# Kernel tuning notes

Hardware: AMD Instinct MI355X
Metric: run time of the kernel (lower is better)

## Reference

```python
import jax, jax.numpy as jnp
import numpy as np

N_NODES = 50000
N_EDGES = 800000
IN_DIM = 6
HID = 256
OUT = 256
N_EXPERTS = 8
N_LAYERS = 2
N_GRAPHS = 64


def setup_inputs() -> dict:
    key = jax.random.key(0)
    ks = jax.random.split(key, 16)
    s = 0.05
    x = jax.random.normal(ks[0], (N_NODES, IN_DIM), dtype=jnp.float32)
    edge_index = jax.random.randint(ks[1], (2, N_EDGES), 0, N_NODES, dtype=jnp.int64)
    batch = jnp.sort(jax.random.randint(ks[2], (N_NODES,), 0, N_GRAPHS, dtype=jnp.int64))
    # shared encoder
    W_enc = jax.random.normal(ks[3], (IN_DIM, HID), jnp.float32) * s
    b_enc = jnp.zeros((HID,), jnp.float32)
    # router MLP: (HID+2) -> HID -> N_EXPERTS
    Wr1 = jax.random.normal(ks[4], (HID + 2, HID), jnp.float32) * s
    br1 = jnp.zeros((HID,), jnp.float32)
    Wr2 = jax.random.normal(ks[5], (HID, N_EXPERTS), jnp.float32) * s
    br2 = jnp.zeros((N_EXPERTS,), jnp.float32)
    # experts: 2 GraphConv layers each (self weight + neighbor weight + bias), stacked over experts
    Ws0 = jax.random.normal(ks[6], (N_EXPERTS, HID, HID), jnp.float32) * s
    Wn0 = jax.random.normal(ks[7], (N_EXPERTS, HID, HID), jnp.float32) * s
    b0 = jnp.zeros((N_EXPERTS, HID), jnp.float32)
    Ws1 = jax.random.normal(ks[8], (N_EXPERTS, HID, OUT), jnp.float32) * s
    Wn1 = jax.random.normal(ks[9], (N_EXPERTS, HID, OUT), jnp.float32) * s
    b1 = jnp.zeros((N_EXPERTS, OUT), jnp.float32)
    return dict(x=x, edge_index=edge_index, batch=batch, W_enc=W_enc, b_enc=b_enc,
                Wr1=Wr1, br1=br1, Wr2=Wr2, br2=br2,
                Ws0=Ws0, Wn0=Wn0, b0=b0, Ws1=Ws1, Wn1=Wn1, b1=b1)


def _graph_conv(h, src, dst, Ws, Wn, b):
    # PyG GraphConv: x' = x @ Ws + sum_{j in N(i)} x_j @ Wn + b
    msg = h[src] @ Wn                                   # [E, d_out]
    agg = jax.ops.segment_sum(msg, dst, num_segments=N_NODES)
    return h @ Ws + agg + b


def reference(x, edge_index, batch, W_enc, b_enc, Wr1, br1, Wr2, br2,
              Ws0, Wn0, b0, Ws1, Wn1, b1):
    src, dst = edge_index[0], edge_index[1]
    # shared encoder
    h = jax.nn.relu(x @ W_enc + b_enc)                  # [N, HID]
    # graph size features: per-graph node count and edge count, log-scaled, broadcast to nodes
    ones_n = jnp.ones((h.shape[0],), h.dtype)
    node_cnt = jax.ops.segment_sum(ones_n, batch, num_segments=N_GRAPHS)
    edge_cnt = jax.ops.segment_sum(jnp.ones((src.shape[0],), h.dtype), batch[src], num_segments=N_GRAPHS)
    size_feat = jnp.stack([jnp.log1p(node_cnt)[batch], jnp.log1p(edge_cnt)[batch]], axis=-1)  # [N, 2]
    # router -> top-1 expert index
    r = jax.nn.relu(jnp.concatenate([h, size_feat], axis=-1) @ Wr1 + br1)
    logits = r @ Wr2 + br2                              # [N, n_experts]
    idx = jnp.argmax(logits, axis=-1)                   # [N]
    # dense compute-all-experts, then gather by argmax (faithful to original)
    out = jnp.zeros((h.shape[0], Ws1.shape[-1]), h.dtype)
    for e in range(N_EXPERTS):
        z = jax.nn.relu(_graph_conv(h, src, dst, Ws0[e], Wn0[e], b0[e]))
        y_e = _graph_conv(z, src, dst, Ws1[e], Wn1[e], b1[e])   # [N, OUT]
        out = out + jnp.where((idx == e)[:, None], y_e, 0.0)
    return out
```

## Files before the change

kernel.cpp:

```cpp
#include <hip/hip_runtime.h>
#include <hip/hip_bf16.h>
#include <math.h>

#define NN 50000
#define NE 800000
#define NG 64
#define NEXP 8

typedef __attribute__((ext_vector_type(8))) short bf16x8;
typedef __attribute__((ext_vector_type(4))) float f32x4;
typedef unsigned short ushort_t;

__device__ __forceinline__ unsigned short f2bf(float f) {
  union { float f; unsigned u; } x; x.f = f;
  unsigned r = x.u + 0x7fff + ((x.u >> 16) & 1);
  return (unsigned short)(r >> 16);
}
__device__ __forceinline__ float bf2f(unsigned short u) {
  union { unsigned u; float f; } x; x.u = ((unsigned)u) << 16; return x.f;
}

__device__ __forceinline__ void gld16(const void* g, void* l) {
  __builtin_amdgcn_global_load_lds(
      (const __attribute__((address_space(1))) unsigned int*)g,
      (__attribute__((address_space(3))) unsigned int*)l, 16, 0, 0);
}

__global__ __launch_bounds__(256) void k_encoder(
    const float* __restrict__ x, const float* __restrict__ W,
    const float* __restrict__ b, ushort_t* __restrict__ Xb,
    ushort_t* __restrict__ Xlo) {
  int i = blockIdx.x, n = threadIdx.x;
  float acc = b[n];
#pragma unroll
  for (int k = 0; k < 6; k++) acc = fmaf(x[i * 6 + k], W[k * 256 + n], acc);
  acc = fmaxf(acc, 0.f);
  unsigned short hb = f2bf(acc);
  Xb[(size_t)i * 512 + n] = hb;
  Xlo[(size_t)i * 256 + n] = f2bf(acc - bf2f(hb));
}

__global__ __launch_bounds__(256) void k_count_nodes(
    const int* __restrict__ batch, int* __restrict__ node_cnt) {
  __shared__ int bins[NG];
  int t = threadIdx.x;
  if (t < NG) bins[t] = 0;
  __syncthreads();
  for (int i = blockIdx.x * blockDim.x + t; i < NN; i += gridDim.x * blockDim.x)
    atomicAdd(&bins[batch[i]], 1);
  __syncthreads();
  if (t < NG) atomicAdd(&node_cnt[t], bins[t]);
}

__global__ __launch_bounds__(256) void k_count_edges(
    const int* __restrict__ ei, const int* __restrict__ batch,
    int* __restrict__ edge_cnt, int* __restrict__ deg) {
  __shared__ int bins[NG];
  int t = threadIdx.x;
  if (t < NG) bins[t] = 0;
  __syncthreads();
  for (int e = blockIdx.x * blockDim.x + t; e < NE; e += gridDim.x * blockDim.x) {
    int s = ei[e];
    int d = ei[NE + e];
    atomicAdd(&bins[batch[s]], 1);
    atomicAdd(&deg[d], 1);
  }
  __syncthreads();
  if (t < NG) atomicAdd(&edge_cnt[t], bins[t]);
}

__global__ __launch_bounds__(256) void k_sizefeat(
    const int* __restrict__ batch, const int* __restrict__ node_cnt,
    const int* __restrict__ edge_cnt, float* __restrict__ sf0,
    float* __restrict__ sf1) {
  int i = blockIdx.x * blockDim.x + threadIdx.x;
  if (i < NN) {
    int g = batch[i];
    sf0[i] = log1pf((float)node_cnt[g]);
    sf1[i] = log1pf((float)edge_cnt[g]);
  }
}

__global__ __launch_bounds__(1024) void k_scan(
    const int* __restrict__ deg, int* __restrict__ offs, int* __restrict__ cursor) {
  __shared__ int wsums[16];
  int t = threadIdx.x, lane = t & 63, wid = t >> 6;
  int carry = 0;
  for (int base = 0; base < NN; base += 1024) {
    int i = base + t;
    int v = (i < NN) ? deg[i] : 0;
    int x = v;
#pragma unroll
    for (int d = 1; d < 64; d <<= 1) {
      int y = __shfl_up(x, d, 64);
      if (lane >= d) x += y;
    }
    if (lane == 63) wsums[wid] = x;
    __syncthreads();
    if (wid == 0) {
      int s = (lane < 16) ? wsums[lane] : 0;
#pragma unroll
      for (int d = 1; d < 16; d <<= 1) {
        int y = __shfl_up(s, d, 64);
        if (lane >= d) s += y;
      }
      if (lane < 16) wsums[lane] = s;
    }
    __syncthreads();
    int wpre = (wid > 0) ? wsums[wid - 1] : 0;
    int excl = carry + wpre + x - v;
    if (i < NN) { offs[i] = excl; cursor[i] = excl; }
    int btot = wsums[15];
    __syncthreads();
    carry += btot;
  }
  if (t == 0) offs[NN] = carry;
}

__global__ __launch_bounds__(256) void k_fill_csr(
    const int* __restrict__ ei, int* __restrict__ cursor, int* __restrict__ edge_src) {
  int e = blockIdx.x * blockDim.x + threadIdx.x;
  if (e < NE) {
    int d = ei[NE + e];
    int pos = atomicAdd(&cursor[d], 1);
    edge_src[pos] = ei[e];
  }
}

__global__ __launch_bounds__(256) void k_agg_h2(
    const int* __restrict__ offs, const int* __restrict__ edge_src,
    ushort_t* __restrict__ Xb) {
  int wid = threadIdx.x >> 6, lane = threadIdx.x & 63;
  int half = lane >> 5, cl = lane & 31;
  int i = blockIdx.x * 4 + wid;
  if (i >= NN) return;
  int e0 = offs[i], e1 = offs[i + 1];
  float acc[8] = {};
  int k = e0;
  for (; k + 8 <= e1; k += 8) {
    int s0 = edge_src[k + half];
    int s1 = edge_src[k + 2 + half];
    int s2 = edge_src[k + 4 + half];
    int s3 = edge_src[k + 6 + half];
    bf16x8 v0 = *(const bf16x8*)&Xb[(size_t)s0 * 512 + cl * 8];
    bf16x8 v1 = *(const bf16x8*)&Xb[(size_t)s1 * 512 + cl * 8];
    bf16x8 v2 = *(const bf16x8*)&Xb[(size_t)s2 * 512 + cl * 8];
    bf16x8 v3 = *(const bf16x8*)&Xb[(size_t)s3 * 512 + cl * 8];
#pragma unroll
    for (int j = 0; j < 8; j++) acc[j] += bf2f((unsigned short)v0[j]);
#pragma unroll
    for (int j = 0; j < 8; j++) acc[j] += bf2f((unsigned short)v1[j]);
#pragma unroll
    for (int j = 0; j < 8; j++) acc[j] += bf2f((unsigned short)v2[j]);
#pragma unroll
    for (int j = 0; j < 8; j++) acc[j] += bf2f((unsigned short)v3[j]);
  }
  for (; k + 2 <= e1; k += 2) {
    int s0 = edge_src[k + half];
    bf16x8 v0 = *(const bf16x8*)&Xb[(size_t)s0 * 512 + cl * 8];
#pragma unroll
    for (int j = 0; j < 8; j++) acc[j] += bf2f((unsigned short)v0[j]);
  }
  if (k < e1 && half == 0) {
    int s0 = edge_src[k];
    bf16x8 v0 = *(const bf16x8*)&Xb[(size_t)s0 * 512 + cl * 8];
#pragma unroll
    for (int j = 0; j < 8; j++) acc[j] += bf2f((unsigned short)v0[j]);
  }
#pragma unroll
  for (int j = 0; j < 8; j++) acc[j] += __shfl_xor(acc[j], 32, 64);
  if (half == 0) {
    bf16x8 o;
#pragma unroll
    for (int j = 0; j < 8; j++) o[j] = (short)f2bf(acc[j]);
    *(bf16x8*)(&Xb[(size_t)i * 512 + 256 + cl * 8]) = o;
  }
}

__global__ __launch_bounds__(256) void k_prep_w(
    const float* __restrict__ Ws0, const float* __restrict__ Wn0,
    const float* __restrict__ Ws1, const float* __restrict__ Wn1,
    ushort_t* __restrict__ Wt1, ushort_t* __restrict__ Wt2) {
  __shared__ float tile[32][33];
  int z = blockIdx.z;
  int e = z & 7;
  const float* Ws = (z < 8) ? Ws0 : Ws1;
  const float* Wn = (z < 8) ? Wn0 : Wn1;
  ushort_t* Wt = (z < 8) ? Wt1 : Wt2;
  int kt = blockIdx.x;
  int nt = blockIdx.y;
  int tx = threadIdx.x & 31, ty = threadIdx.x >> 5;
  const float* src = (kt < 8) ? (Ws + e * 65536 + (kt * 32) * 256)
                              : (Wn + e * 65536 + ((kt - 8) * 32) * 256);
#pragma unroll
  for (int rr = 0; rr < 32; rr += 8) {
    int k = rr + ty;
    tile[k][tx] = src[k * 256 + nt * 32 + tx];
  }
  __syncthreads();
#pragma unroll
  for (int rr = 0; rr < 32; rr += 8) {
    int n = rr + ty;
    Wt[(size_t)e * 131072 + (nt * 32 + n) * 512 + kt * 32 + tx] = f2bf(tile[tx][n]);
  }
}

__global__ __launch_bounds__(256) void k_prep_wr1(
    const float* __restrict__ Wr1, ushort_t* __restrict__ Wr1t) {
  int k = blockIdx.x;
  int n = threadIdx.x;
  unsigned short v;
  if (k < 256) {
    v = f2bf(Wr1[k * 256 + n]);
  } else {
    float f = Wr1[(k - 256) * 256 + n];
    unsigned short h = f2bf(f);
    v = f2bf(f - bf2f(h));
  }
  Wr1t[(size_t)n * 512 + k] = v;
}

#define TIE_TAU 1e-4f
__global__ __launch_bounds__(256) void k_router_mfma(
    const ushort_t* __restrict__ Xb,
    const ushort_t* __restrict__ Xlo,
    const ushort_t* __restrict__ Wr1t,
    const float* __restrict__ Wr1, const float* __restrict__ br1,
    const float* __restrict__ Wr2, const float* __restrict__ sf0,
    const float* __restrict__ sf1, float* __restrict__ Lpart) {
  __shared__ ushort_t As[2][4096];
  __shared__ ushort_t Bs1[2][4096];
  __shared__ ushort_t Bs2[2][4096];
  __shared__ float Lsm[128][NEXP];
  int t = threadIdx.x;
  int w = t >> 6, lane = t & 63;
  int m0 = blockIdx.x * 128;
  int n0 = blockIdx.y * 128;
  int wm = w >> 1, wn = w & 1;
  for (int z = t; z < 128 * NEXP; z += 256) ((float*)Lsm)[z] = 0.f;

  auto STAGE = [&](int s, int kt) {
    int k0 = (kt & 7) * 32;
    bool hi = kt < 8;
#pragma unroll
    for (int i = 0; i < 2; i++) {
      int c = w * 128 + i * 64 + lane;
      int r = c >> 2, kc = c & 3;
      int gr = m0 + r; if (gr >= NN) gr = NN - 1;
      int dst = (w * 128 + i * 64) * 8;
      if (hi) {
        gld16(Xb + (size_t)gr * 512 + k0 + kc * 8, (void*)&As[s][dst]);
        gld16(Wr1t + (size_t)(n0 + r) * 512 + k0 + kc * 8, (void*)&Bs1[s][dst]);
        gld16(Wr1t + (size_t)(n0 + r) * 512 + 256 + k0 + kc * 8, (void*)&Bs2[s][dst]);
      } else {
        gld16(Xlo + (size_t)gr * 256 + k0 + kc * 8, (void*)&As[s][dst]);
        gld16(Wr1t + (size_t)(n0 + r) * 512 + k0 + kc * 8, (void*)&Bs1[s][dst]);
      }
    }
  };

  f32x4 acc[4][4] = {};
  STAGE(0, 0);
  __syncthreads();
  for (int kt = 0; kt < 16; kt++) {
    int cur = kt & 1;
    if (kt < 15) STAGE(cur ^ 1, kt + 1);
    bf16x8 a[4], b1[4];
#pragma unroll
    for (int i = 0; i < 4; i++) {
      int ra = wm * 64 + i * 16 + (lane & 15);
      a[i] = *(const bf16x8*)&As[cur][ra * 32 + (lane >> 4) * 8];
      int nb = wn * 64 + i * 16 + (lane & 15);
      b1[i] = *(const bf16x8*)&Bs1[cur][nb * 32 + (lane >> 4) * 8];
    }
#pragma unroll
    for (int i = 0; i < 4; i++)
#pragma unroll
      for (int j = 0; j < 4; j++)
        acc[i][j] = __builtin_amdgcn_mfma_f32_16x16x32_bf16(a[i], b1[j], acc[i][j], 0, 0, 0);
    if (kt < 8) {
      bf16x8 b2[4];
#pragma unroll
      for (int i = 0; i < 4; i++) {
        int nb = wn * 64 + i * 16 + (lane & 15);
        b2[i] = *(const bf16x8*)&Bs2[cur][nb * 32 + (lane >> 4) * 8];
      }
#pragma unroll
      for (int i = 0; i < 4; i++)
#pragma unroll
        for (int j = 0; j < 4; j++)
          acc[i][j] = __builtin_amdgcn_mfma_f32_16x16x32_bf16(a[i], b2[j], acc[i][j], 0, 0, 0);
    }
    __syncthreads();
  }

  int q = lane >> 4, c15 = lane & 15;
  float bb[4], w6[4], w7[4];
#pragma unroll
  for (int j = 0; j < 4; j++) {
    int col = n0 + wn * 64 + j * 16 + c15;
    bb[j] = br1[col];
    w6[j] = Wr1[65536 + col];
    w7[j] = Wr1[65792 + col];
  }
#pragma unroll
  for (int i = 0; i < 4; i++)
#pragma unroll
    for (int v = 0; v < 4; v++) {
      int row = m0 + wm * 64 + i * 16 + q * 4 + v;
      float s0v = (row < NN) ? sf0[row] : 0.f;
      float s1v = (row < NN) ? sf1[row] : 0.f;
#pragma unroll
      for (int j = 0; j < 4; j++)
        acc[i][j][v] = fmaxf(acc[i][j][v] + bb[j] + s0v * w6[j] + s1v * w7[j], 0.f);
    }
#pragma unroll
  for (int e = 0; e < NEXP; e++) {
    float wr2j[4];
#pragma unroll
    for (int j = 0; j < 4; j++)
      wr2j[j] = Wr2[(n0 + wn * 64 + j * 16 + c15) * 8 + e];
    float pe[4][4];
#pragma unroll
    for (int i = 0; i < 4; i++)
#pragma unroll
      for (int v = 0; v < 4; v++) {
        float s = acc[i][0][v] * wr2j[0];
        s = fmaf(acc[i][1][v], wr2j[1], s);
        s = fmaf(acc[i][2][v], wr2j[2], s);
        s = fmaf(acc[i][3][v], wr2j[3], s);
        pe[i][v] = s;
      }
#pragma unroll
    for (int d = 1; d < 16; d <<= 1)
#pragma unroll
      for (int i = 0; i < 4; i++)
#pragma unroll
        for (int v = 0; v < 4; v++)
          pe[i][v] += __shfl_xor(pe[i][v], d, 64);
    if (c15 == 0) {
#pragma unroll
      for (int i = 0; i < 4; i++)
#pragma unroll
        for (int v = 0; v < 4; v++)
          atomicAdd(&Lsm[wm * 64 + i * 16 + q * 4 + v][e], pe[i][v]);
    }
  }
  __syncthreads();
  for (int z = t; z < 128 * NEXP; z += 256) {
    int lr = z >> 3, e = z & 7;
    int row = m0 + lr;
    if (row < NN)
      Lpart[(size_t)blockIdx.y * NN * 8 + (size_t)row * 8 + e] = Lsm[lr][e];
  }
}

__global__ __launch_bounds__(256) void k_argmax(
    const float* __restrict__ Lpart, const float* __restrict__ br2,
    int* __restrict__ idx, int* __restrict__ nfix, int* __restrict__ fixlist) {
  int i = blockIdx.x * 256 + threadIdx.x;
  if (i >= NN) return;
  float best = -1e30f, second = -1e30f; int bi = 0;
#pragma unroll
  for (int e = 0; e < NEXP; e++) {
    float v = Lpart[(size_t)i * 8 + e] + Lpart[(size_t)NN * 8 + (size_t)i * 8 + e]
              + br2[e];
    if (v > best) { second = best; best = v; bi = e; }
    else if (v > second) second = v;
  }
  idx[i] = bi;
  if (best - second < TIE_TAU) {
    int p = atomicAdd(nfix, 1);
    fixlist[p] = i;
  }
}

__global__ __launch_bounds__(256) void k_fixup(
    const float* __restrict__ x, const float* __restrict__ W_enc,
    const float* __restrict__ b_enc, const float* __restrict__ Wr1,
    const float* __restrict__ br1, const float* __restrict__ Wr2,
    const float* __restrict__ br2, const float* __restrict__ sf0,
    const float* __restrict__ sf1, const int* __restrict__ fixlist,
    const int* __restrict__ nfix, int* __restrict__ idx) {
  __shared__ float hsh[256];
  __shared__ float lred[4][NEXP];
  int n = *nfix;
  int t = threadIdx.x, wid = t >> 6, lane = t & 63;
  for (int qq = blockIdx.x; qq < n; qq += gridDim.x) {
    int node = fixlist[qq];
    float hv = b_enc[t];
#pragma unroll
    for (int k = 0; k < 6; k++)
      hv = fmaf(x[node * 6 + k], W_enc[k * 256 + t], hv);
    hsh[t] = fmaxf(hv, 0.f);
    __syncthreads();
    float acc = br1[t] + sf0[node] * Wr1[65536 + t] + sf1[node] * Wr1[65792 + t];
    for (int k = 0; k < 256; k++)
      acc = fmaf(hsh[k], Wr1[k * 256 + t], acc);
    float r = fmaxf(acc, 0.f);
    float le[NEXP];
#pragma unroll
    for (int e = 0; e < NEXP; e++) le[e] = r * Wr2[t * 8 + e];
#pragma unroll
    for (int d = 32; d > 0; d >>= 1)
#pragma unroll
      for (int e = 0; e < NEXP; e++) le[e] += __shfl_xor(le[e], d, 64);
    if (lane == 0) {
#pragma unroll
      for (int e = 0; e < NEXP; e++) lred[wid][e] = le[e];
    }
    __syncthreads();
    if (t == 0) {
      float best = -1e30f; int bi = 0;
      for (int e = 0; e < NEXP; e++) {
        float v = lred[0][e] + lred[1][e] + lred[2][e] + lred[3][e] + br2[e];
        if (v > best) { best = v; bi = e; }
      }
      idx[node] = bi;
    }
    __syncthreads();
  }
}

__global__ __launch_bounds__(256) void k_ecnt(
    const int* __restrict__ idx, int* __restrict__ ecnt) {
  __shared__ int bins[NEXP];
  int t = threadIdx.x;
  if (t < NEXP) bins[t] = 0;
  __syncthreads();
  for (int i = blockIdx.x * 256 + t; i < NN; i += gridDim.x * 256)
    atomicAdd(&bins[idx[i]], 1);
  __syncthreads();
  if (t < NEXP) atomicAdd(&ecnt[t], bins[t]);
}

__global__ __launch_bounds__(256) void k_srcmask(
    const int* __restrict__ ei, const int* __restrict__ idx,
    unsigned int* __restrict__ mask) {
  int k = blockIdx.x * 256 + threadIdx.x;
  if (k < NE) {
    int s = ei[k], d = ei[NE + k];
    atomicOr(&mask[s], 1u << idx[d]);
  }
  if (k < NN) atomicOr(&mask[k], 1u << idx[k]);
}

__global__ __launch_bounds__(256) void k_scount(
    const unsigned int* __restrict__ mask, int* __restrict__ scnt) {
  __shared__ int bins[NEXP];
  int t = threadIdx.x;
  if (t < NEXP) bins[t] = 0;
  __syncthreads();
  for (int i = blockIdx.x * 256 + t; i < NN; i += gridDim.x * 256) {
    unsigned m = mask[i];
    while (m) { int b = __ffs(m) - 1; atomicAdd(&bins[b], 1); m &= m - 1; }
  }
  __syncthreads();
  if (t < NEXP) atomicAdd(&scnt[t], bins[t]);
}

__global__ void k_bucket_offs(const int* __restrict__ ecnt,
                              const int* __restrict__ scnt,
                              int* __restrict__ boff, int* __restrict__ bcur,
                              int* __restrict__ tstart,
                              int* __restrict__ soff, int* __restrict__ scur) {
  if (threadIdx.x == 0) {
    int s = 0, ts = 0, s2 = 0;
    for (int e = 0; e < NEXP; e++) {
      boff[e] = s; bcur[e] = s;
      tstart[e] = ts;
      ts += (ecnt[e] + 127) / 128;
      s += ecnt[e];
      soff[e] = s2; scur[e] = s2;
      s2 += scnt[e];
    }
    boff[NEXP] = s;
    tstart[NEXP] = ts;
    soff[NEXP] = s2;
  }
}

#define BF_BLOCKS 64
__global__ __launch_bounds__(256) void k_bucket_fill2(
    const int* __restrict__ idx, int* __restrict__ bcur, int* __restrict__ nlist) {
  __shared__ int lcnt[NEXP];
  __shared__ int lbase[NEXP];
  int t = threadIdx.x;
  int chunk = (NN + BF_BLOCKS - 1) / BF_BLOCKS;
  int lo = blockIdx.x * chunk;
  int hi = lo + chunk; if (hi > NN) hi = NN;
  if (t < NEXP) lcnt[t] = 0;
  __syncthreads();
  for (int i = lo + t; i < hi; i += 256) atomicAdd(&lcnt[idx[i]], 1);
  __syncthreads();
  if (t < NEXP) lbase[t] = atomicAdd(&bcur[t], lcnt[t]);
  __syncthreads();
  if (t < NEXP) lcnt[t] = 0;
  __syncthreads();
  for (int i = lo + t; i < hi; i += 256) {
    int e = idx[i];
    int p = atomicAdd(&lcnt[e], 1);
    nlist[lbase[e] + p] = i;
  }
}

__global__ __launch_bounds__(256) void k_scompact(
    const unsigned int* __restrict__ mask, int* __restrict__ scur,
    int* __restrict__ slist) {
  __shared__ int lcnt[NEXP];
  __shared__ int lbase[NEXP];
  int t = threadIdx.x;
  int chunk = (NN + BF_BLOCKS - 1) / BF_BLOCKS;
  int lo = blockIdx.x * chunk;
  int hi = lo + chunk; if (hi > NN) hi = NN;
  if (t < NEXP) lcnt[t] = 0;
  __syncthreads();
  for (int i = lo + t; i < hi; i += 256) {
    unsigned m = mask[i];
    while (m) { int b = __ffs(m) - 1; atomicAdd(&lcnt[b], 1); m &= m - 1; }
  }
  __syncthreads();
  if (t < NEXP) lbase[t] = atomicAdd(&scur[t], lcnt[t]);
  __syncthreads();
  if (t < NEXP) lcnt[t] = 0;
  __syncthreads();
  for (int i = lo + t; i < hi; i += 256) {
    unsigned m = mask[i];
    while (m) {
      int b = __ffs(m) - 1;
      int p = atomicAdd(&lcnt[b], 1);
      slist[lbase[b] + p] = i;
      m &= m - 1;
    }
  }
}

__global__ __launch_bounds__(256) void k_layer1_rows(
    const ushort_t* __restrict__ Abf,
    const ushort_t* __restrict__ Wt,
    const float* __restrict__ b0, const int* __restrict__ idx,
    const int* __restrict__ slist, const int* __restrict__ soff, int e,
    ushort_t* __restrict__ Zb, ushort_t* __restrict__ A2) {
  int base = soff[e];
  int cnt = soff[e + 1] - base;
  int m0 = blockIdx.x * 128;
  if (m0 >= cnt) return;
  __shared__ ushort_t As[2][4096];
  __shared__ ushort_t Bs[2][4096];
  __shared__ int rows[128];
  __shared__ int sidx[128];
  int t = threadIdx.x;
  if (t < 128) {
    int r = (m0 + t < cnt) ? slist[base + m0 + t] : -1;
    rows[t] = r;
    sidx[t] = (r >= 0) ? idx[r] : -1;
  }
  __syncthreads();
  int w = t >> 6, lane = t & 63;
  int n0 = blockIdx.y * 128;
  int wm = w >> 1, wn = w & 1;
  const ushort_t* Wb = Wt + (size_t)e * 131072;

  auto STAGE = [&](int s, int kt) {
    int k0 = kt * 32;
#pragma unroll
    for (int i = 0; i < 2; i++) {
      int c = w * 128 + i * 64 + lane;
      int r = c >> 2, kc = c & 3;
      int nd = rows[r]; if (nd < 0) nd = 0;
      int dst = (w * 128 + i * 64) * 8;
      gld16(Abf + (size_t)nd * 512 + k0 + kc * 8, (void*)&As[s][dst]);
      gld16(Wb + (size_t)(n0 + r) * 512 + k0 + kc * 8, (void*)&Bs[s][dst]);
    }
  };

  f32x4 acc[4][4] = {};
  STAGE(0, 0);
  __syncthreads();
  for (int kt = 0; kt < 16; kt++) {
    int cur = kt & 1;
    if (kt < 15) STAGE(cur ^ 1, kt + 1);
    bf16x8 a[4], b[4];
#pragma unroll
    for (int i = 0; i < 4; i++) {
      int ra = wm * 64 + i * 16 + (lane & 15);
      a[i] = *(const bf16x8*)&As[cur][ra * 32 + (lane >> 4) * 8];
      int nb = wn * 64 + i * 16 + (lane & 15);
      b[i] = *(const bf16x8*)&Bs[cur][nb * 32 + (lane >> 4) * 8];
    }
#pragma unroll
    for (int i = 0; i < 4; i++)
#pragma unroll
      for (int j = 0; j < 4; j++)
        acc[i][j] = __builtin_amdgcn_mfma_f32_16x16x32_bf16(a[i], b[j], acc[i][j], 0, 0, 0);
    __syncthreads();
  }
  int q = lane >> 4, c15 = lane & 15;
#pragma unroll
  for (int i = 0; i < 4; i++) {
#pragma unroll
    for (int j = 0; j < 4; j++) {
      int col = n0 + wn * 64 + j * 16 + c15;
      float bias = b0[e * 256 + col];
#pragma unroll
      for (int v = 0; v < 4; v++) {
        int lrow = wm * 64 + i * 16 + q * 4 + v;
        int node = rows[lrow];
        if (node >= 0) {
          unsigned short zb = f2bf(fmaxf(acc[i][j][v] + bias, 0.f));
          Zb[(size_t)node * 256 + col] = zb;
          if (sidx[lrow] == e) A2[(size_t)node * 512 + col] = zb;
        }
      }
    }
  }
}

__global__ __launch_bounds__(256) void k_agg_z2(
    const ushort_t* __restrict__ Zb, const int* __restrict__ offs,
    const int* __restrict__ edge_src, const int* __restrict__ nlist,
    const int* __restrict__ boff, int e, ushort_t* __restrict__ A2) {
  int wid = threadIdx.x >> 6, lane = threadIdx.x & 63;
  int half = lane >> 5, cl = lane & 31;
  int base = boff[e];
  int cnt = boff[e + 1] - base;
  for (int b = blockIdx.x * 4 + wid; b < cnt; b += gridDim.x * 4) {
    int i = nlist[base + b];
    int e0 = offs[i], e1 = offs[i + 1];
    float acc[8] = {};
    int k = e0;
    for (; k + 8 <= e1; k += 8) {
      int s0 = edge_src[k + half];
      int s1 = edge_src[k + 2 + half];
      int s2 = edge_src[k + 4 + half];
      int s3 = edge_src[k + 6 + half];
      bf16x8 v0 = *(const bf16x8*)&Zb[(size_t)s0 * 256 + cl * 8];
      bf16x8 v1 = *(const bf16x8*)&Zb[(size_t)s1 * 256 + cl * 8];
      bf16x8 v2 = *(const bf16x8*)&Zb[(size_t)s2 * 256 + cl * 8];
      bf16x8 v3 = *(const bf16x8*)&Zb[(size_t)s3 * 256 + cl * 8];
#pragma unroll
      for (int j = 0; j < 8; j++) acc[j] += bf2f((unsigned short)v0[j]);
#pragma unroll
      for (int j = 0; j < 8; j++) acc[j] += bf2f((unsigned short)v1[j]);
#pragma unroll
      for (int j = 0; j < 8; j++) acc[j] += bf2f((unsigned short)v2[j]);
#pragma unroll
      for (int j = 0; j < 8; j++) acc[j] += bf2f((unsigned short)v3[j]);
    }
    for (; k + 2 <= e1; k += 2) {
      int s0 = edge_src[k + half];
      bf16x8 v0 = *(const bf16x8*)&Zb[(size_t)s0 * 256 + cl * 8];
#pragma unroll
      for (int j = 0; j < 8; j++) acc[j] += bf2f((unsigned short)v0[j]);
    }
    if (k < e1 && half == 0) {
      int s0 = edge_src[k];
      bf16x8 v0 = *(const bf16x8*)&Zb[(size_t)s0 * 256 + cl * 8];
#pragma unroll
      for (int j = 0; j < 8; j++) acc[j] += bf2f((unsigned short)v0[j]);
    }
#pragma unroll
    for (int j = 0; j < 8; j++) acc[j] += __shfl_xor(acc[j], 32, 64);
    if (half == 0) {
      bf16x8 o;
#pragma unroll
      for (int j = 0; j < 8; j++) o[j] = (short)f2bf(acc[j]);
      *(bf16x8*)(&A2[(size_t)i * 512 + 256 + cl * 8]) = o;
    }
  }
}

#define MAXT2 (391 + NEXP)
__global__ __launch_bounds__(256) void k_layer2_mfma(
    const ushort_t* __restrict__ A2,
    const ushort_t* __restrict__ Wt,
    const float* __restrict__ b1, const int* __restrict__ nlist,
    const int* __restrict__ boff, const int* __restrict__ tstart,
    float* __restrict__ outp) {
  __shared__ ushort_t As[2][4096];
  __shared__ ushort_t Bs[2][4096];
  __shared__ int rows[128];
  int t = threadIdx.x;
  int tx = blockIdx.x;
  int e = -1;
#pragma unroll
  for (int q = 0; q < NEXP; q++)
    if (tx >= tstart[q] && tx < tstart[q + 1]) e = q;
  if (e < 0) return;
  int tile = tx - tstart[e];
  int base = boff[e];
  int cnt = boff[e + 1] - base;
  int m0 = tile * 128;
  if (t < 128) rows[t] = (m0 + t < cnt) ? nlist[base + m0 + t] : -1;
  __syncthreads();
  int w = t >> 6, lane = t & 63;
  int n0 = blockIdx.y * 128;
  int wm = w >> 1, wn = w & 1;
  const ushort_t* Wb = Wt + (size_t)e * 131072;

  auto STAGE = [&](int s, int kt) {
    int k0 = kt * 32;
#pragma unroll
    for (int i = 0; i < 2; i++) {
      int c = w * 128 + i * 64 + lane;
      int r = c >> 2, kc = c & 3;
      int nd = rows[r]; if (nd < 0) nd = 0;
      int dst = (w * 128 + i * 64) * 8;
      gld16(A2 + (size_t)nd * 512 + k0 + kc * 8, (void*)&As[s][dst]);
      gld16(Wb + (size_t)(n0 + r) * 512 + k0 + kc * 8, (void*)&Bs[s][dst]);
    }
  };

  f32x4 acc[4][4] = {};
  STAGE(0, 0);
  __syncthreads();
  for (int kt = 0; kt < 16; kt++) {
    int cur = kt & 1;
    if (kt < 15) STAGE(cur ^ 1, kt + 1);
    bf16x8 a[4], b[4];
#pragma unroll
    for (int i = 0; i < 4; i++) {
      int ra = wm * 64 + i * 16 + (lane & 15);
      a[i] = *(const bf16x8*)&As[cur][ra * 32 + (lane >> 4) * 8];
      int nb = wn * 64 + i * 16 + (lane & 15);
      b[i] = *(const bf16x8*)&Bs[cur][nb * 32 + (lane >> 4) * 8];
    }
#pragma unroll
    for (int i = 0; i < 4; i++)
#pragma unroll
      for (int j = 0; j < 4; j++)
        acc[i][j] = __builtin_amdgcn_mfma_f32_16x16x32_bf16(a[i], b[j], acc[i][j], 0, 0, 0);
    __syncthreads();
  }
  int q = lane >> 4, c15 = lane & 15;
#pragma unroll
  for (int i = 0; i < 4; i++) {
#pragma unroll
    for (int j = 0; j < 4; j++) {
      int col = n0 + wn * 64 + j * 16 + c15;
      float bias = b1[e * 256 + col];
#pragma unroll
      for (int v = 0; v < 4; v++) {
        int lrow = wm * 64 + i * 16 + q * 4 + v;
        int node = rows[lrow];
        if (node >= 0) outp[(size_t)node * 256 + col] = acc[i][j][v] + bias;
      }
    }
  }
}

static inline char* wsalloc(char*& p, size_t bytes) {
  char* r = p;
  p += (bytes + 255) & ~(size_t)255;
  return r;
}

extern "C" void kernel_launch(void* const* d_in, const int* in_sizes, int n_in,
                              void* d_out, int out_size, void* d_ws, size_t ws_size,
                              hipStream_t stream) {
  const float* x     = (const float*)d_in[0];
  const int*   ei    = (const int*)d_in[1];
  const int*   batch = (const int*)d_in[2];
  const float* W_enc = (const float*)d_in[3];
  const float* b_enc = (const float*)d_in[4];
  const float* Wr1   = (const float*)d_in[5];
  const float* br1   = (const float*)d_in[6];
  const float* Wr2   = (const float*)d_in[7];
  const float* br2   = (const float*)d_in[8];
  const float* Ws0   = (const float*)d_in[9];
  const float* Wn0   = (const float*)d_in[10];
  const float* b0    = (const float*)d_in[11];
  const float* Ws1   = (const float*)d_in[12];
  const float* Wn1   = (const float*)d_in[13];
  const float* b1    = (const float*)d_in[14];
  float* outp = (float*)d_out;

  char* p = (char*)d_ws;
  ushort_t* Xb   = (ushort_t*)wsalloc(p, (size_t)NN * 512 * 2);
  ushort_t* Zb   = (ushort_t*)wsalloc(p, (size_t)NN * 256 * 2);
  ushort_t* A2   = (ushort_t*)wsalloc(p, (size_t)NN * 512 * 2);
  ushort_t* Xlo  = Zb;
  float*    Lpart= (float*)wsalloc(p, (size_t)2 * NN * 8 * 4);
  ushort_t* Wt1  = (ushort_t*)wsalloc(p, (size_t)NEXP * 256 * 512 * 2);
  ushort_t* Wt2  = (ushort_t*)wsalloc(p, (size_t)NEXP * 256 * 512 * 2);
  ushort_t* Wr1t = (ushort_t*)wsalloc(p, (size_t)256 * 512 * 2);
  int* edge_src  = (int*)wsalloc(p, (size_t)NE * 4);
  int* offs      = (int*)wsalloc(p, (size_t)(NN + 1) * 4);
  int* cursor    = (int*)wsalloc(p, (size_t)NN * 4);
  int* deg       = (int*)wsalloc(p, (size_t)NN * 4);
  int* idxb      = (int*)wsalloc(p, (size_t)NN * 4);
  float* sf0     = (float*)wsalloc(p, (size_t)NN * 4);
  float* sf1     = (float*)wsalloc(p, (size_t)NN * 4);
  int* nlist     = (int*)wsalloc(p, (size_t)NN * 4);
  int* fixlist   = (int*)wsalloc(p, (size_t)NN * 4);
  unsigned int* maskb = (unsigned int*)wsalloc(p, (size_t)NN * 4);
  int* slist     = (int*)wsalloc(p, (size_t)NN * NEXP * 4);
  int* smallb    = (int*)wsalloc(p, 256 * 4);
  int* node_cnt = smallb;
  int* edge_cnt = smallb + 64;
  int* ecnt     = smallb + 128;
  int* boff     = smallb + 136;
  int* bcur     = smallb + 152;
  int* tstart   = smallb + 160;
  int* nfix     = smallb + 192;
  int* scnt     = smallb + 200;
  int* soff     = smallb + 208;
  int* scur     = smallb + 224;

  hipMemsetAsync(deg, 0, (size_t)NN * 4, stream);
  hipMemsetAsync(smallb, 0, 256 * 4, stream);
  hipMemsetAsync(maskb, 0, (size_t)NN * 4, stream);

  k_encoder<<<NN, 256, 0, stream>>>(x, W_enc, b_enc, Xb, Xlo);
  k_count_nodes<<<64, 256, 0, stream>>>(batch, node_cnt);
  k_count_edges<<<128, 256, 0, stream>>>(ei, batch, edge_cnt, deg);
  k_sizefeat<<<(NN + 255) / 256, 256, 0, stream>>>(batch, node_cnt, edge_cnt, sf0, sf1);
  k_scan<<<1, 1024, 0, stream>>>(deg, offs, cursor);
  k_fill_csr<<<(NE + 255) / 256, 256, 0, stream>>>(ei, cursor, edge_src);
  k_agg_h2<<<(NN + 3) / 4, 256, 0, stream>>>(offs, edge_src, Xb);
  k_prep_w<<<dim3(16, 8, 16), 256, 0, stream>>>(Ws0, Wn0, Ws1, Wn1, Wt1, Wt2);
  k_prep_wr1<<<512, 256, 0, stream>>>(Wr1, Wr1t);
  k_router_mfma<<<dim3((NN + 127) / 128, 2), 256, 0, stream>>>(
      Xb, Xlo, Wr1t, Wr1, br1, Wr2, sf0, sf1, Lpart);
  k_argmax<<<(NN + 255) / 256, 256, 0, stream>>>(Lpart, br2, idxb, nfix, fixlist);
  k_fixup<<<256, 256, 0, stream>>>(x, W_enc, b_enc, Wr1, br1, Wr2, br2,
                                   sf0, sf1, fixlist, nfix, idxb);
  k_srcmask<<<(NE + 255) / 256, 256, 0, stream>>>(ei, idxb, maskb);
  k_ecnt<<<64, 256, 0, stream>>>(idxb, ecnt);
  k_scount<<<64, 256, 0, stream>>>(maskb, scnt);
  k_bucket_offs<<<1, 64, 0, stream>>>(ecnt, scnt, boff, bcur, tstart, soff, scur);
  k_bucket_fill2<<<BF_BLOCKS, 256, 0, stream>>>(idxb, bcur, nlist);
  k_scompact<<<BF_BLOCKS, 256, 0, stream>>>(maskb, scur, slist);
  for (int e = 0; e < NEXP; e++) {
    k_layer1_rows<<<dim3((NN + 127) / 128, 2), 256, 0, stream>>>(
        Xb, Wt1, b0, idxb, slist, soff, e, Zb, A2);
    k_agg_z2<<<3125, 256, 0, stream>>>(Zb, offs, edge_src, nlist, boff, e, A2);
  }
  k_layer2_mfma<<<dim3(MAXT2, 2), 256, 0, stream>>>(
      A2, Wt2, b1, nlist, boff, tstart, outp);
}
```

Baseline: 645.5 us.

## Restructure router GEMM: resident swizzled weight tile in LDS, A streamed from global

The router kernel now loads a full 64-column slice of the transposed router weight (all K) into LDS once, with an XOR swizzle to avoid bank conflicts. A-operand fragments are read directly from global memory into registers with software double-buffering, which removes the per-k-step LDS staging and barriers. The N split goes from 2 to 4 blocks, so each block does half the columns and argmax sums four partial logit buffers. This trades more redundant reads of the activation rows and a larger partial buffer for fewer syncs and more parallel blocks.

```diff
diff --git a/kernel.cpp b/kernel.cpp
--- a/kernel.cpp
+++ b/kernel.cpp
@@ -228,77 +228,95 @@
     const float* __restrict__ Wr1, const float* __restrict__ br1,
     const float* __restrict__ Wr2, const float* __restrict__ sf0,
     const float* __restrict__ sf1, float* __restrict__ Lpart) {
-  __shared__ ushort_t As[2][4096];
-  __shared__ ushort_t Bs1[2][4096];
-  __shared__ ushort_t Bs2[2][4096];
+  __shared__ ushort_t Bs[64 * 512];
   __shared__ float Lsm[128][NEXP];
   int t = threadIdx.x;
   int w = t >> 6, lane = t & 63;
   int m0 = blockIdx.x * 128;
-  int n0 = blockIdx.y * 128;
+  int n0 = blockIdx.y * 64;
   int wm = w >> 1, wn = w & 1;
+  int q16 = lane >> 4, c15 = lane & 15;
   for (int z = t; z < 128 * NEXP; z += 256) ((float*)Lsm)[z] = 0.f;
 
-  auto STAGE = [&](int s, int kt) {
-    int k0 = (kt & 7) * 32;
-    bool hi = kt < 8;
-#pragma unroll
-    for (int i = 0; i < 2; i++) {
-      int c = w * 128 + i * 64 + lane;
-      int r = c >> 2, kc = c & 3;
-      int gr = m0 + r; if (gr >= NN) gr = NN - 1;
-      int dst = (w * 128 + i * 64) * 8;
-      if (hi) {
-        gld16(Xb + (size_t)gr * 512 + k0 + kc * 8, (void*)&As[s][dst]);
-        gld16(Wr1t + (size_t)(n0 + r) * 512 + k0 + kc * 8, (void*)&Bs1[s][dst]);
-        gld16(Wr1t + (size_t)(n0 + r) * 512 + 256 + k0 + kc * 8, (void*)&Bs2[s][dst]);
-      } else {
-        gld16(Xlo + (size_t)gr * 256 + k0 + kc * 8, (void*)&As[s][dst]);
-        gld16(Wr1t + (size_t)(n0 + r) * 512 + k0 + kc * 8, (void*)&Bs1[s][dst]);
+#pragma unroll
+  for (int r = 0; r < 16; r++) {
+    int C0 = (r * 4 + w) * 64;
+    int C = C0 + lane;
+    int n = C >> 6, c = C & 63;
+    gld16(Wr1t + (size_t)(n0 + n) * 512 + ((c ^ (n & 7)) << 3),
+          (void*)((char*)Bs + (size_t)C0 * 16));
+  }
+
+  const ushort_t* pHi[4];
+  const ushort_t* pLo[4];
+#pragma unroll
+  for (int i = 0; i < 4; i++) {
+    int row = m0 + wm * 64 + i * 16 + c15;
+    if (row >= NN) row = NN - 1;
+    pHi[i] = Xb + (size_t)row * 512 + q16 * 8;
+    pLo[i] = Xlo + (size_t)row * 256 + q16 * 8;
+  }
+
+  f32x4 acc[4][2] = {};
+  __syncthreads();
+
+  auto LOADA_HI = [&](bf16x8* a, int kt) {
+#pragma unroll
+    for (int i = 0; i < 4; i++) a[i] = *(const bf16x8*)(pHi[i] + kt * 32);
+  };
+  auto LOADA_LO = [&](bf16x8* a, int kt) {
+#pragma unroll
+    for (int i = 0; i < 4; i++) a[i] = *(const bf16x8*)(pLo[i] + kt * 32);
+  };
+  auto MFMA_HI = [&](bf16x8* a, int kt) {
+#pragma unroll
+    for (int j = 0; j < 2; j++) {
+      int nb = wn * 32 + j * 16 + c15;
+      const char* brow = (const char*)Bs + nb * 1024;
+      int sw = nb & 7;
+      bf16x8 bh = *(const bf16x8*)(brow + (((kt * 4 + q16) ^ sw) << 4));
+      bf16x8 bl = *(const bf16x8*)(brow + (((32 + kt * 4 + q16) ^ sw) << 4));
+#pragma unroll
+      for (int i = 0; i < 4; i++) {
+        acc[i][j] = __builtin_amdgcn_mfma_f32_16x16x32_bf16(a[i], bh, acc[i][j], 0, 0, 0);
+        acc[i][j] = __builtin_amdgcn_mfma_f32_16x16x32_bf16(a[i], bl, acc[i][j], 0, 0, 0);
       }
     }
   };
-
-  f32x4 acc[4][4] = {};
-  STAGE(0, 0);
-  __syncthreads();
-  for (int kt = 0; kt < 16; kt++) {
-    int cur = kt & 1;
-    if (kt < 15) STAGE(cur ^ 1, kt + 1);
-    bf16x8 a[4], b1[4];
-#pragma unroll
-    for (int i = 0; i < 4; i++) {
-      int ra = wm * 64 + i * 16 + (lane & 15);
-      a[i] = *(const bf16x8*)&As[cur][ra * 32 + (lane >> 4) * 8];
-      int nb = wn * 64 + i * 16 + (lane & 15);
-      b1[i] = *(const bf16x8*)&Bs1[cur][nb * 32 + (lane >> 4) * 8];
-    }
-#pragma unroll
-    for (int i = 0; i < 4; i++)
-#pragma unroll
-      for (int j = 0; j < 4; j++)
-        acc[i][j] = __builtin_amdgcn_mfma_f32_16x16x32_bf16(a[i], b1[j], acc[i][j], 0, 0, 0);
-    if (kt < 8) {
-      bf16x8 b2[4];
-#pragma unroll
-      for (int i = 0; i < 4; i++) {
-        int nb = wn * 64 + i * 16 + (lane & 15);
-        b2[i] = *(const bf16x8*)&Bs2[cur][nb * 32 + (lane >> 4) * 8];
-      }
+  auto MFMA_LO = [&](bf16x8* a, int kt) {
+#pragma unroll
+    for (int j = 0; j < 2; j++) {
+      int nb = wn * 32 + j * 16 + c15;
+      const char* brow = (const char*)Bs + nb * 1024;
+      int sw = nb & 7;
+      bf16x8 bh = *(const bf16x8*)(brow + (((kt * 4 + q16) ^ sw) << 4));
 #pragma unroll
       for (int i = 0; i < 4; i++)
-#pragma unroll
-        for (int j = 0; j < 4; j++)
-          acc[i][j] = __builtin_amdgcn_mfma_f32_16x16x32_bf16(a[i], b2[j], acc[i][j], 0, 0, 0);
-    }
-    __syncthreads();
-  }
-
-  int q = lane >> 4, c15 = lane & 15;
-  float bb[4], w6[4], w7[4];
-#pragma unroll
-  for (int j = 0; j < 4; j++) {
-    int col = n0 + wn * 64 + j * 16 + c15;
+        acc[i][j] = __builtin_amdgcn_mfma_f32_16x16x32_bf16(a[i], bh, acc[i][j], 0, 0, 0);
+    }
+  };
+
+  bf16x8 aA[4], aB[4];
+  LOADA_HI(aA, 0);
+#pragma unroll
+  for (int k2 = 0; k2 < 4; k2++) {
+    LOADA_HI(aB, 2 * k2 + 1);
+    MFMA_HI(aA, 2 * k2);
+    if (k2 < 3) LOADA_HI(aA, 2 * k2 + 2); else LOADA_LO(aA, 0);
+    MFMA_HI(aB, 2 * k2 + 1);
+  }
+#pragma unroll
+  for (int k2 = 0; k2 < 4; k2++) {
+    LOADA_LO(aB, 2 * k2 + 1);
+    MFMA_LO(aA, 2 * k2);
+    if (k2 < 3) LOADA_LO(aA, 2 * k2 + 2);
+    MFMA_LO(aB, 2 * k2 + 1);
+  }
+
+  float bb[2], w6[2], w7[2];
+#pragma unroll
+  for (int j = 0; j < 2; j++) {
+    int col = n0 + wn * 32 + j * 16 + c15;
     bb[j] = br1[col];
     w6[j] = Wr1[65536 + col];
     w7[j] = Wr1[65792 + col];
@@ -307,30 +325,25 @@
   for (int i = 0; i < 4; i++)
 #pragma unroll
     for (int v = 0; v < 4; v++) {
-      int row = m0 + wm * 64 + i * 16 + q * 4 + v;
+      int row = m0 + wm * 64 + i * 16 + q16 * 4 + v;
       float s0v = (row < NN) ? sf0[row] : 0.f;
       float s1v = (row < NN) ? sf1[row] : 0.f;
 #pragma unroll
-      for (int j = 0; j < 4; j++)
+      for (int j = 0; j < 2; j++)
         acc[i][j][v] = fmaxf(acc[i][j][v] + bb[j] + s0v * w6[j] + s1v * w7[j], 0.f);
     }
 #pragma unroll
   for (int e = 0; e < NEXP; e++) {
-    float wr2j[4];
-#pragma unroll
-    for (int j = 0; j < 4; j++)
-      wr2j[j] = Wr2[(n0 + wn * 64 + j * 16 + c15) * 8 + e];
+    float wr2j[2];
+#pragma unroll
+    for (int j = 0; j < 2; j++)
+      wr2j[j] = Wr2[(n0 + wn * 32 + j * 16 + c15) * 8 + e];
     float pe[4][4];
 #pragma unroll
     for (int i = 0; i < 4; i++)
 #pragma unroll
-      for (int v = 0; v < 4; v++) {
-        float s = acc[i][0][v] * wr2j[0];
-        s = fmaf(acc[i][1][v], wr2j[1], s);
-        s = fmaf(acc[i][2][v], wr2j[2], s);
-        s = fmaf(acc[i][3][v], wr2j[3], s);
-        pe[i][v] = s;
-      }
+      for (int v = 0; v < 4; v++)
+        pe[i][v] = fmaf(acc[i][1][v], wr2j[1], acc[i][0][v] * wr2j[0]);
 #pragma unroll
     for (int d = 1; d < 16; d <<= 1)
 #pragma unroll
@@ -343,7 +356,7 @@
       for (int i = 0; i < 4; i++)
 #pragma unroll
         for (int v = 0; v < 4; v++)
-          atomicAdd(&Lsm[wm * 64 + i * 16 + q * 4 + v][e], pe[i][v]);
+          atomicAdd(&Lsm[wm * 64 + i * 16 + q16 * 4 + v][e], pe[i][v]);
     }
   }
   __syncthreads();
@@ -351,7 +364,7 @@
     int lr = z >> 3, e = z & 7;
     int row = m0 + lr;
     if (row < NN)
-      Lpart[(size_t)blockIdx.y * NN * 8 + (size_t)row * 8 + e] = Lsm[lr][e];
+      Lpart[(size_t)blockIdx.y * (NN * 8) + (size_t)row * 8 + e] = Lsm[lr][e];
   }
 }
 
@@ -363,8 +376,10 @@
   float best = -1e30f, second = -1e30f; int bi = 0;
 #pragma unroll
   for (int e = 0; e < NEXP; e++) {
-    float v = Lpart[(size_t)i * 8 + e] + Lpart[(size_t)NN * 8 + (size_t)i * 8 + e]
-              + br2[e];
+    float v = br2[e];
+#pragma unroll
+    for (int s = 0; s < 4; s++)
+      v += Lpart[(size_t)s * (NN * 8) + (size_t)i * 8 + e];
     if (v > best) { second = best; best = v; bi = e; }
     else if (v > second) second = v;
   }
@@ -780,7 +795,7 @@
   ushort_t* Zb   = (ushort_t*)wsalloc(p, (size_t)NN * 256 * 2);
   ushort_t* A2   = (ushort_t*)wsalloc(p, (size_t)NN * 512 * 2);
   ushort_t* Xlo  = Zb;
-  float*    Lpart= (float*)wsalloc(p, (size_t)2 * NN * 8 * 4);
+  float*    Lpart= (float*)wsalloc(p, (size_t)4 * NN * 8 * 4);
   ushort_t* Wt1  = (ushort_t*)wsalloc(p, (size_t)NEXP * 256 * 512 * 2);
   ushort_t* Wt2  = (ushort_t*)wsalloc(p, (size_t)NEXP * 256 * 512 * 2);
   ushort_t* Wr1t = (ushort_t*)wsalloc(p, (size_t)256 * 512 * 2);
@@ -820,7 +835,7 @@
   k_agg_h2<<<(NN + 3) / 4, 256, 0, stream>>>(offs, edge_src, Xb);
   k_prep_w<<<dim3(16, 8, 16), 256, 0, stream>>>(Ws0, Wn0, Ws1, Wn1, Wt1, Wt2);
   k_prep_wr1<<<512, 256, 0, stream>>>(Wr1, Wr1t);
-  k_router_mfma<<<dim3((NN + 127) / 128, 2), 256, 0, stream>>>(
+  k_router_mfma<<<dim3((NN + 127) / 128, 4), 256, 0, stream>>>(
       Xb, Xlo, Wr1t, Wr1, br1, Wr2, sf0, sf1, Lpart);
   k_argmax<<<(NN + 255) / 256, 256, 0, stream>>>(Lpart, br2, idxb, nfix, fixlist);
   k_fixup<<<256, 256, 0, stream>>>(x, W_enc, b_enc, Wr1, br1, Wr2, br2,
```

Result: slower. 678.6 us (+5.1%).
